# Performance work log

Hardware: AMD Instinct MI355X
Metric: run time of the kernel (lower is better)

Reference implementation:

```python
import jax, jax.numpy as jnp
import numpy as np

NEG_SLOPE = 0.2
LN_EPS = 1e-6

B, L, D, H = 32, 512, 256, 4
N = B * L
E = 65536
C = D  # per-head out channels (GATConv out_channels=d_model)


def setup_inputs() -> dict:
    key = jax.random.key(0)
    ks = jax.random.split(key, 10)
    s = 1.0 / np.sqrt(D)
    inputs = jax.random.normal(ks[0], (B, L, D), dtype=jnp.float32)
    edge_index = jax.random.randint(ks[1], (2, E), 0, N, dtype=jnp.int64)
    return {
        "inputs": inputs,
        "edge_index": edge_index,
        "ln_gamma": jnp.ones((D,), jnp.float32),
        "ln_beta": jnp.zeros((D,), jnp.float32),
        "W1": jax.random.normal(ks[2], (D, D), jnp.float32) * s,   # linear_before_gnn
        "b1": jnp.zeros((D,), jnp.float32),
        "W_gat": jax.random.normal(ks[3], (H * C, D), jnp.float32) * s,  # GATConv.lin (no bias)
        "att_src": jax.random.normal(ks[4], (H, C), jnp.float32) * s,
        "att_dst": jax.random.normal(ks[5], (H, C), jnp.float32) * s,
        "bias_gat": jnp.zeros((C,), jnp.float32),  # concat=False -> size out_channels
        "W2": jax.random.normal(ks[6], (D, D), jnp.float32) * s,   # linear_after_gnn
        "b2": jnp.zeros((D,), jnp.float32),
    }


def _gat_conv(x, edge_index, W_gat, att_src, att_dst, bias_gat):
    # x: [N, D] -> project to [N, H, C]
    xh = (x @ W_gat.T).reshape(N, H, C)
    # add self loops (PyG default add_self_loops=True)
    loops = jnp.arange(N, dtype=edge_index.dtype)
    src = jnp.concatenate([edge_index[0], loops])  # message source j
    dst = jnp.concatenate([edge_index[1], loops])  # message target i
    # per-node attention logits [N, H]
    a_src = jnp.einsum("nhc,hc->nh", xh, att_src)
    a_dst = jnp.einsum("nhc,hc->nh", xh, att_dst)
    # per-edge logits and segment softmax over destination node
    e = jax.nn.leaky_relu(a_src[src] + a_dst[dst], NEG_SLOPE)  # [Etot, H]
    e_max = jax.ops.segment_max(e, dst, num_segments=N)        # every node has a self loop
    e = jnp.exp(e - e_max[dst])
    denom = jax.ops.segment_sum(e, dst, num_segments=N)
    alpha = e / denom[dst]                                     # [Etot, H]
    # weighted message aggregation (dropout on alpha skipped: eval mode)
    msg = xh[src] * alpha[:, :, None]                          # [Etot, H, C]
    out = jax.ops.segment_sum(msg, dst, num_segments=N)        # [N, H, C]
    return out.mean(axis=1) + bias_gat                         # concat=False -> head mean


def reference(inputs, edge_index, ln_gamma, ln_beta, W1, b1, W_gat, att_src, att_dst, bias_gat, W2, b2):
    # LayerNorm(eps=1e-6)
    mu = inputs.mean(-1, keepdims=True)
    var = jnp.mean((inputs - mu) ** 2, axis=-1, keepdims=True)
    x = (inputs - mu) * jax.lax.rsqrt(var + LN_EPS) * ln_gamma + ln_beta
    x = x.reshape(-1, D)
    gnn_in = x @ W1.T + b1
    gnn_out = _gat_conv(gnn_in, edge_index, W_gat, att_src, att_dst, bias_gat)
    y = gnn_out @ W2.T + b2
    # dropout is identity in eval mode; residual add
    return y.reshape(B, L, D) + inputs
```

## Files before the change

kernel.cpp:

```cpp
#include <hip/hip_runtime.h>
#include <math.h>

#define N_NODES 16384
#define D_MODEL 256
#define H_HEADS 4
#define C_CH 256
#define E_EDGES 65536
#define ETOT (E_EDGES + N_NODES)
#define HC 1024
#define MAXDEG 64
#define PSZ 262144

typedef __bf16 bf16x8 __attribute__((ext_vector_type(8)));
typedef __bf16 bf16x4 __attribute__((ext_vector_type(4)));
typedef float f32x4 __attribute__((ext_vector_type(4)));

__device__ __forceinline__ __bf16 f2bf(float f) { return (__bf16)f; }
__device__ __forceinline__ float bf2f(__bf16 b) { return (float)b; }

__global__ __launch_bounds__(256) void prep1_ln(
    const float* __restrict__ Wg, const float* __restrict__ att_src,
    const float* __restrict__ att_dst, const float* __restrict__ W2,
    const int* __restrict__ ei, const float* __restrict__ in,
    const float* __restrict__ gamma, const float* __restrict__ beta,
    float* __restrict__ t, float* __restrict__ Vp, int* __restrict__ cnt,
    int* __restrict__ csr, __bf16* __restrict__ x_ln)
{
    int b = blockIdx.x;
    int tid = threadIdx.x;
    if (b >= 2432) {
        int wave = tid >> 6, lane = tid & 63;
        int row = (b - 2432) * 4 + wave;
        float4 v = ((const float4*)(in + (size_t)row * D_MODEL))[lane];
        float s  = v.x + v.y + v.z + v.w;
        float sq = v.x*v.x + v.y*v.y + v.z*v.z + v.w*v.w;
        for (int off = 32; off; off >>= 1) {
            s  += __shfl_xor(s,  off);
            sq += __shfl_xor(sq, off);
        }
        float mean = s * (1.0f / D_MODEL);
        float var  = sq * (1.0f / D_MODEL) - mean * mean;
        float inv  = rsqrtf(var + 1e-6f);
        float4 g = ((const float4*)gamma)[lane];
        float4 bb = ((const float4*)beta)[lane];
        bf16x4 o;
        o[0] = f2bf((v.x - mean) * inv * g.x + bb.x);
        o[1] = f2bf((v.y - mean) * inv * g.y + bb.y);
        o[2] = f2bf((v.z - mean) * inv * g.z + bb.z);
        o[3] = f2bf((v.w - mean) * inv * g.w + bb.w);
        *(bf16x4*)(x_ln + (size_t)row * D_MODEL + lane * 4) = o;
        return;
    }
    if (b < 64) {
        int v = b >> 3, sl = b & 7, h = v & 3;
        const float* att = ((v < 4) ? att_src : att_dst) + h * C_CH;
        float acc = 0.f;
        #pragma unroll
        for (int j = 0; j < 32; ++j) {
            int c = sl * 32 + j;
            acc = fmaf(Wg[(size_t)(h * 256 + c) * 256 + tid], att[c], acc);
        }
        atomicAdd(&t[v * 256 + tid], acc);
        return;
    }
    if (b < 2112) {
        int bb2 = b - 64;
        int orig = bb2 >> 3, cs = bb2 & 7;
        int og = (orig & 63) * 4, h = orig >> 6;
        const float* w2r = W2 + (size_t)og * 256;
        const float* wgp = Wg + ((size_t)h * 256) * 256 + tid;
        float a0 = 0.f, a1 = 0.f, a2 = 0.f, a3 = 0.f;
        int cb = cs * 32;
        #pragma unroll 4
        for (int c = cb; c < cb + 32; ++c) {
            float wv = wgp[(size_t)c * 256];
            a0 = fmaf(w2r[c],       wv, a0);
            a1 = fmaf(w2r[256 + c], wv, a1);
            a2 = fmaf(w2r[512 + c], wv, a2);
            a3 = fmaf(w2r[768 + c], wv, a3);
        }
        size_t base = (size_t)cs * PSZ + (size_t)og * 1024 + h * 256 + tid;
        Vp[base]        = a0;
        Vp[base + 1024] = a1;
        Vp[base + 2048] = a2;
        Vp[base + 3072] = a3;
        return;
    }
    {
        int e = (b - 2112) * 256 + tid;
        int src, dst;
        if (e < E_EDGES) { src = ei[e]; dst = ei[E_EDGES + e]; }
        else             { src = dst = e - E_EDGES; }
        int pos = atomicAdd(cnt + dst, 1);
        csr[(size_t)dst * MAXDEG + pos] = src;
    }
}

__global__ __launch_bounds__(256) void prep2(
    const float* __restrict__ t, const float* __restrict__ W1,
    const float* __restrict__ b1, const float* __restrict__ Vp,
    const float* __restrict__ W2, const float* __restrict__ bg,
    const float* __restrict__ b2, float* __restrict__ u2,
    float* __restrict__ c0, float* __restrict__ Wzp,
    float* __restrict__ bias_z)
{
    __shared__ float red[4][4];
    __shared__ float vsh[4][32];
    int b = blockIdx.x;
    int d = threadIdx.x;

    if (b < 2048) {
        int orig = b >> 3, ks = b & 7;
        int og = (orig & 63) * 4, h = orig >> 6;
        int lane = d & 63, wid = d >> 6;
        int kb = ks * 32;
        size_t vbase = (size_t)og * 1024 + h * 256;

        if (d < 128) {
            int j = d >> 5, kk = d & 31;
            float s = 0.f;
            #pragma unroll
            for (int cs = 0; cs < 8; ++cs)
                s += Vp[(size_t)cs * PSZ + vbase + (size_t)j * 1024 + kb + kk];
            vsh[j][kk] = s;
        }
        __syncthreads();

        float a0 = 0.f, a1 = 0.f, a2 = 0.f, a3 = 0.f;
        #pragma unroll 4
        for (int k = 0; k < 32; ++k) {
            float w1v = W1[(size_t)(kb + k) * 256 + d];
            a0 = fmaf(vsh[0][k], w1v, a0);
            a1 = fmaf(vsh[1][k], w1v, a1);
            a2 = fmaf(vsh[2][k], w1v, a2);
            a3 = fmaf(vsh[3][k], w1v, a3);
        }
        size_t base = (size_t)ks * PSZ + vbase + d;
        Wzp[base]        = a0;
        Wzp[base + 1024] = a1;
        Wzp[base + 2048] = a2;
        Wzp[base + 3072] = a3;

        if (ks == 0) {
            float b1v = b1[d];
            #pragma unroll
            for (int j = 0; j < 4; ++j) {
                float vsum = 0.f;
                #pragma unroll
                for (int cs = 0; cs < 8; ++cs)
                    vsum += Vp[(size_t)cs * PSZ + vbase + (size_t)j * 1024 + d];
                float p = vsum * b1v;
                for (int s = 32; s; s >>= 1) p += __shfl_xor(p, s);
                if (lane == 0) red[j][wid] = p;
            }
            __syncthreads();
            if (d < 4) {
                float s = red[d][0] + red[d][1] + red[d][2] + red[d][3];
                atomicAdd(&bias_z[og + d], 0.25f * s);
            }
            if (h == 0) {
                __syncthreads();
                float bgv = bg[d];
                #pragma unroll
                for (int j = 0; j < 4; ++j) {
                    float q = W2[(size_t)(og + j) * 256 + d] * bgv;
                    for (int s = 32; s; s >>= 1) q += __shfl_xor(q, s);
                    if (lane == 0) red[j][wid] = q;
                }
                __syncthreads();
                if (d < 4) {
                    float s = red[d][0] + red[d][1] + red[d][2] + red[d][3];
                    atomicAdd(&bias_z[og + d], s + b2[og + d]);
                }
            }
        }
        return;
    }
    {
        int bb = b - 2048;
        int v = bb >> 3, sl = bb & 7;
        const float* tv = t + v * 256;
        float acc = 0.f;
        #pragma unroll
        for (int j = 0; j < 32; ++j) {
            int k = sl * 32 + j;
            acc = fmaf(tv[k], W1[(size_t)k * 256 + d], acc);
        }
        atomicAdd(&u2[v * 256 + d], acc);
        if (d < 32) {
            float p = tv[sl * 32 + d] * b1[sl * 32 + d];
            for (int s = 16; s; s >>= 1) p += __shfl_xor(p, s);
            if (d == 0) atomicAdd(&c0[v], p);
        }
    }
}

__global__ __launch_bounds__(256) void logits_cvt(
    const __bf16* __restrict__ x_ln, const float* __restrict__ u2,
    const float* __restrict__ c0, float* __restrict__ a_src,
    float* __restrict__ a_dst, const float* __restrict__ Wzp,
    __bf16* __restrict__ Wz)
{
    int b = blockIdx.x;
    int tid = threadIdx.x;
    if (b >= 4096) {
        int idx = (b - 4096) * 256 + tid;
        float4 v = make_float4(0.f, 0.f, 0.f, 0.f);
        #pragma unroll
        for (int p = 0; p < 8; ++p) {
            float4 t4 = ((const float4*)(Wzp + (size_t)p * PSZ))[idx];
            v.x += t4.x; v.y += t4.y; v.z += t4.z; v.w += t4.w;
        }
        bf16x4 o;
        o[0] = f2bf(v.x); o[1] = f2bf(v.y); o[2] = f2bf(v.z); o[3] = f2bf(v.w);
        *(bf16x4*)(Wz + (size_t)idx * 4) = o;
        return;
    }
    __shared__ float u2s[8][256];
    __shared__ float c0s[8];
    #pragma unroll
    for (int k = 0; k < 8; ++k) u2s[k][tid] = u2[k * 256 + tid];
    if (tid < 8) c0s[tid] = c0[tid];
    __syncthreads();

    int wave = tid >> 6, lane = tid & 63;
    int n = b * 4 + wave;
    int v = lane >> 3, p = lane & 7;
    const __bf16* xp = x_ln + (size_t)n * D_MODEL + p * 32;
    const float*  up = &u2s[v][p * 32];
    float acc = 0.f;
    #pragma unroll
    for (int ti = 0; ti < 4; ++ti) {
        bf16x8 x = *(const bf16x8*)(xp + ti * 8);
        #pragma unroll
        for (int j = 0; j < 8; ++j)
            acc = fmaf(bf2f(x[j]), up[ti * 8 + j], acc);
    }
    acc += __shfl_xor(acc, 1);
    acc += __shfl_xor(acc, 2);
    acc += __shfl_xor(acc, 4);
    if (p == 0) {
        float o = acc + c0s[v];
        if (v < 4) a_src[n * H_HEADS + v] = o;
        else       a_dst[n * H_HEADS + (v - 4)] = o;
    }
}

__global__ __launch_bounds__(256) void gat_fused(
    const __bf16* __restrict__ x_ln, const float* __restrict__ a_src,
    const float* __restrict__ a_dst, const int* __restrict__ cnt,
    const int* __restrict__ csr, __bf16* __restrict__ agg)
{
    int wave = threadIdx.x >> 6, lane = threadIdx.x & 63;
    int i = blockIdx.x * 4 + wave;
    int deg = cnt[i];
    int sidx = csr[(size_t)i * MAXDEG + lane];
    float4 ad = *(const float4*)(a_dst + i * H_HEADS);

    float acc[4][4] = {};
    float sm0 = 0.f, sm1 = 0.f, sm2 = 0.f, sm3 = 0.f;

    int e = 0;
    for (; e + 4 <= deg; e += 4) {
        int s0 = __shfl(sidx, e);
        int s1 = __shfl(sidx, e + 1);
        int s2 = __shfl(sidx, e + 2);
        int s3 = __shfl(sidx, e + 3);
        float4 A0 = *(const float4*)(a_src + s0 * H_HEADS);
        float4 A1 = *(const float4*)(a_src + s1 * H_HEADS);
        float4 A2 = *(const float4*)(a_src + s2 * H_HEADS);
        float4 A3 = *(const float4*)(a_src + s3 * H_HEADS);
        bf16x4 X0 = *(const bf16x4*)(x_ln + (size_t)s0 * D_MODEL + lane * 4);
        bf16x4 X1 = *(const bf16x4*)(x_ln + (size_t)s1 * D_MODEL + lane * 4);
        bf16x4 X2 = *(const bf16x4*)(x_ln + (size_t)s2 * D_MODEL + lane * 4);
        bf16x4 X3 = *(const bf16x4*)(x_ln + (size_t)s3 * D_MODEL + lane * 4);

        float l[4][4] = {
            {A0.x + ad.x, A0.y + ad.y, A0.z + ad.z, A0.w + ad.w},
            {A1.x + ad.x, A1.y + ad.y, A1.z + ad.z, A1.w + ad.w},
            {A2.x + ad.x, A2.y + ad.y, A2.z + ad.z, A2.w + ad.w},
            {A3.x + ad.x, A3.y + ad.y, A3.z + ad.z, A3.w + ad.w}};
        float wgt[4][4];
        #pragma unroll
        for (int q = 0; q < 4; ++q)
            #pragma unroll
            for (int h = 0; h < 4; ++h) {
                float lv = l[q][h];
                lv = (lv > 0.f) ? lv : 0.2f * lv;
                wgt[q][h] = __expf(lv);
            }
        sm0 += wgt[0][0] + wgt[1][0] + wgt[2][0] + wgt[3][0];
        sm1 += wgt[0][1] + wgt[1][1] + wgt[2][1] + wgt[3][1];
        sm2 += wgt[0][2] + wgt[1][2] + wgt[2][2] + wgt[3][2];
        sm3 += wgt[0][3] + wgt[1][3] + wgt[2][3] + wgt[3][3];
        #pragma unroll
        for (int j = 0; j < 4; ++j) {
            float x0 = bf2f(X0[j]), x1 = bf2f(X1[j]);
            float x2 = bf2f(X2[j]), x3 = bf2f(X3[j]);
            #pragma unroll
            for (int h = 0; h < 4; ++h) {
                float a = acc[h][j];
                a = fmaf(wgt[0][h], x0, a);
                a = fmaf(wgt[1][h], x1, a);
                a = fmaf(wgt[2][h], x2, a);
                a = fmaf(wgt[3][h], x3, a);
                acc[h][j] = a;
            }
        }
    }
    for (; e < deg; ++e) {
        int s = __shfl(sidx, e);
        float4 as = *(const float4*)(a_src + s * H_HEADS);
        bf16x4 x = *(const bf16x4*)(x_ln + (size_t)s * D_MODEL + lane * 4);
        float l0 = as.x + ad.x, l1 = as.y + ad.y,
              l2 = as.z + ad.z, l3 = as.w + ad.w;
        l0 = (l0 > 0.f) ? l0 : 0.2f * l0;
        l1 = (l1 > 0.f) ? l1 : 0.2f * l1;
        l2 = (l2 > 0.f) ? l2 : 0.2f * l2;
        l3 = (l3 > 0.f) ? l3 : 0.2f * l3;
        float w0 = __expf(l0), w1 = __expf(l1);
        float w2 = __expf(l2), w3 = __expf(l3);
        sm0 += w0; sm1 += w1; sm2 += w2; sm3 += w3;
        #pragma unroll
        for (int j = 0; j < 4; ++j) {
            float xv = bf2f(x[j]);
            acc[0][j] = fmaf(w0, xv, acc[0][j]);
            acc[1][j] = fmaf(w1, xv, acc[1][j]);
            acc[2][j] = fmaf(w2, xv, acc[2][j]);
            acc[3][j] = fmaf(w3, xv, acc[3][j]);
        }
    }
    float sc[4] = {0.25f / sm0, 0.25f / sm1, 0.25f / sm2, 0.25f / sm3};
    #pragma unroll
    for (int h = 0; h < 4; ++h) {
        bf16x4 o;
        #pragma unroll
        for (int j = 0; j < 4; ++j) o[j] = f2bf(acc[h][j] * sc[h]);
        *(bf16x4*)(agg + (size_t)i * HC + h * 256 + lane * 4) = o;
    }
}

#define APAD 72

__global__ __launch_bounds__(512) void gemm_skinny(
    const __bf16* __restrict__ A, const __bf16* __restrict__ B,
    const float* __restrict__ bias, const float* __restrict__ resid,
    float* __restrict__ outf, int K)
{
    __shared__ __align__(16) __bf16 As[64 * APAD];
    __shared__ __align__(16) __bf16 Bs[256 * APAD];
    int tid  = threadIdx.x;
    int lane = tid & 63;
    int w    = tid >> 6;
    int quad = lane >> 4;
    int l16  = lane & 15;
    int m0 = blockIdx.x * 64;
    int n0 = w * 32;

    int srow = tid >> 3, sp = tid & 7;
    const __bf16* Ab = A + (size_t)(m0 + srow) * K + sp * 8;
    const __bf16* Bb = B + (size_t)srow * K + sp * 8;
    size_t rstride = (size_t)64 * K;

    f32x4 acc[4][2] = {};

    bf16x8 a0_, b0_[4];
    bf16x8 a1_, b1_[4];

    auto compute = [&]() {
        #pragma unroll
        for (int ks = 0; ks < 2; ++ks) {
            bf16x8 af[4], bfr[2];
            #pragma unroll
            for (int mt = 0; mt < 4; ++mt)
                af[mt] = *(const bf16x8*)(As + (mt * 16 + l16) * APAD
                                          + ks * 32 + quad * 8);
            #pragma unroll
            for (int nt = 0; nt < 2; ++nt)
                bfr[nt] = *(const bf16x8*)(Bs + (n0 + nt * 16 + l16) * APAD
                                           + ks * 32 + quad * 8);
            #pragma unroll
            for (int mt = 0; mt < 4; ++mt)
                #pragma unroll
                for (int nt = 0; nt < 2; ++nt)
                    acc[mt][nt] = __builtin_amdgcn_mfma_f32_16x16x32_bf16(
                        af[mt], bfr[nt], acc[mt][nt], 0, 0, 0);
        }
    };

    a0_ = *(const bf16x8*)(Ab);
    #pragma unroll
    for (int t = 0; t < 4; ++t)
        b0_[t] = *(const bf16x8*)(Bb + t * rstride);

    for (int kb = 0; kb < K; kb += 128) {
        {
            const __bf16* Ap = Ab + kb + 64;
            const __bf16* Bp = Bb + kb + 64;
            a1_ = *(const bf16x8*)(Ap);
            #pragma unroll
            for (int t = 0; t < 4; ++t)
                b1_[t] = *(const bf16x8*)(Bp + t * rstride);
        }
        __syncthreads();
        *(bf16x8*)(As + srow * APAD + sp * 8) = a0_;
        #pragma unroll
        for (int t = 0; t < 4; ++t)
            *(bf16x8*)(Bs + (srow + t * 64) * APAD + sp * 8) = b0_[t];
        __syncthreads();
        compute();

        if (kb + 128 < K) {
            const __bf16* Ap = Ab + kb + 128;
            const __bf16* Bp = Bb + kb + 128;
            a0_ = *(const bf16x8*)(Ap);
            #pragma unroll
            for (int t = 0; t < 4; ++t)
                b0_[t] = *(const bf16x8*)(Bp + t * rstride);
        }
        __syncthreads();
        *(bf16x8*)(As + srow * APAD + sp * 8) = a1_;
        #pragma unroll
        for (int t = 0; t < 4; ++t)
            *(bf16x8*)(Bs + (srow + t * 64) * APAD + sp * 8) = b1_[t];
        __syncthreads();
        compute();
    }

    #pragma unroll
    for (int nt = 0; nt < 2; ++nt) {
        int col = n0 + nt * 16 + l16;
        float bv = bias[col];
        #pragma unroll
        for (int mt = 0; mt < 4; ++mt) {
            int row = m0 + mt * 16 + quad * 4;
            #pragma unroll
            for (int r = 0; r < 4; ++r) {
                size_t off = (size_t)(row + r) * C_CH + col;
                outf[off] = acc[mt][nt][r] + bv + resid[off];
            }
        }
    }
}

extern "C" void kernel_launch(void* const* d_in, const int* in_sizes, int n_in,
                              void* d_out, int out_size, void* d_ws, size_t ws_size,
                              hipStream_t stream)
{
    const float* inp      = (const float*)d_in[0];
    const int*   ei       = (const int*)  d_in[1];
    const float* ln_gamma = (const float*)d_in[2];
    const float* ln_beta  = (const float*)d_in[3];
    const float* W1       = (const float*)d_in[4];
    const float* b1       = (const float*)d_in[5];
    const float* W_gat    = (const float*)d_in[6];
    const float* att_src  = (const float*)d_in[7];
    const float* att_dst  = (const float*)d_in[8];
    const float* bias_gat = (const float*)d_in[9];
    const float* W2       = (const float*)d_in[10];
    const float* b2       = (const float*)d_in[11];

    char* ws = (char*)d_ws;
    __bf16* x_ln_bf = (__bf16*)(ws);
    __bf16* agg_bf  = (__bf16*)(ws + (8ull  << 20));
    __bf16* Wz_b    = (__bf16*)(ws + (40ull << 20));
    float*  a_src_b = (float*)(ws + (41ull << 20));
    float*  a_dst_b = a_src_b + (size_t)N_NODES * H_HEADS;
    float*  t_vec   = (float*)(ws + (42ull << 20));
    float*  u2      = t_vec + 2048;
    float*  c0      = u2 + 2048;
    float*  bias_z  = c0 + 8;
    int*    cnt     = (int*)(bias_z + 256);
    int*    csr     = (int*)(ws + (45ull << 20));
    float*  Vp      = (float*)(ws + (49ull << 20));
    float*  Wzp     = (float*)(ws + (57ull << 20));

    size_t zbytes = (2048 + 2048 + 8 + 256) * sizeof(float)
                  + N_NODES * sizeof(int);
    hipMemsetAsync(t_vec, 0, zbytes, stream);

    prep1_ln<<<2432 + 4096, 256, 0, stream>>>(W_gat, att_src, att_dst, W2, ei,
                                              inp, ln_gamma, ln_beta,
                                              t_vec, Vp, cnt, csr, x_ln_bf);
    prep2<<<2112, 256, 0, stream>>>(t_vec, W1, b1, Vp, W2, bias_gat, b2,
                                    u2, c0, Wzp, bias_z);
    logits_cvt<<<4096 + 256, 256, 0, stream>>>(x_ln_bf, u2, c0,
                                               a_src_b, a_dst_b, Wzp, Wz_b);
    gat_fused<<<N_NODES / 4, 256, 0, stream>>>(x_ln_bf, a_src_b, a_dst_b,
                                               cnt, csr, agg_bf);
    gemm_skinny<<<N_NODES / 64, 512, 0, stream>>>(agg_bf, Wz_b, bias_z, inp,
                                                  (float*)d_out, HC);
}
```

Baseline: 155.5 us.

## Parallelize GAT edge weights across lanes and halve split-K partials in prep

```diff
diff --git a/kernel.cpp b/kernel.cpp
--- a/kernel.cpp
+++ b/kernel.cpp
@@ -28,9 +28,9 @@
 {
     int b = blockIdx.x;
     int tid = threadIdx.x;
-    if (b >= 2432) {
+    if (b >= 1408) {
         int wave = tid >> 6, lane = tid & 63;
-        int row = (b - 2432) * 4 + wave;
+        int row = (b - 1408) * 4 + wave;
         float4 v = ((const float4*)(in + (size_t)row * D_MODEL))[lane];
         float s  = v.x + v.y + v.z + v.w;
         float sq = v.x*v.x + v.y*v.y + v.z*v.z + v.w*v.w;
@@ -63,16 +63,16 @@
         atomicAdd(&t[v * 256 + tid], acc);
         return;
     }
-    if (b < 2112) {
+    if (b < 1088) {
         int bb2 = b - 64;
-        int orig = bb2 >> 3, cs = bb2 & 7;
+        int orig = bb2 >> 2, cs = bb2 & 3;
         int og = (orig & 63) * 4, h = orig >> 6;
         const float* w2r = W2 + (size_t)og * 256;
         const float* wgp = Wg + ((size_t)h * 256) * 256 + tid;
         float a0 = 0.f, a1 = 0.f, a2 = 0.f, a3 = 0.f;
-        int cb = cs * 32;
+        int cb = cs * 64;
         #pragma unroll 4
-        for (int c = cb; c < cb + 32; ++c) {
+        for (int c = cb; c < cb + 64; ++c) {
             float wv = wgp[(size_t)c * 256];
             a0 = fmaf(w2r[c],       wv, a0);
             a1 = fmaf(w2r[256 + c], wv, a1);
@@ -87,7 +87,7 @@
         return;
     }
     {
-        int e = (b - 2112) * 256 + tid;
+        int e = (b - 1088) * 256 + tid;
         int src, dst;
         if (e < E_EDGES) { src = ei[e]; dst = ei[E_EDGES + e]; }
         else             { src = dst = e - E_EDGES; }
@@ -105,22 +105,22 @@
     float* __restrict__ bias_z)
 {
     __shared__ float red[4][4];
-    __shared__ float vsh[4][32];
+    __shared__ float vsh[4][64];
     int b = blockIdx.x;
     int d = threadIdx.x;
 
-    if (b < 2048) {
-        int orig = b >> 3, ks = b & 7;
+    if (b < 1024) {
+        int orig = b >> 2, ks = b & 3;
         int og = (orig & 63) * 4, h = orig >> 6;
         int lane = d & 63, wid = d >> 6;
-        int kb = ks * 32;
+        int kb = ks * 64;
         size_t vbase = (size_t)og * 1024 + h * 256;
 
-        if (d < 128) {
-            int j = d >> 5, kk = d & 31;
+        {
+            int j = d >> 6, kk = d & 63;
             float s = 0.f;
             #pragma unroll
-            for (int cs = 0; cs < 8; ++cs)
+            for (int cs = 0; cs < 4; ++cs)
                 s += Vp[(size_t)cs * PSZ + vbase + (size_t)j * 1024 + kb + kk];
             vsh[j][kk] = s;
         }
@@ -128,7 +128,7 @@
 
         float a0 = 0.f, a1 = 0.f, a2 = 0.f, a3 = 0.f;
         #pragma unroll 4
-        for (int k = 0; k < 32; ++k) {
+        for (int k = 0; k < 64; ++k) {
             float w1v = W1[(size_t)(kb + k) * 256 + d];
             a0 = fmaf(vsh[0][k], w1v, a0);
             a1 = fmaf(vsh[1][k], w1v, a1);
@@ -147,7 +147,7 @@
             for (int j = 0; j < 4; ++j) {
                 float vsum = 0.f;
                 #pragma unroll
-                for (int cs = 0; cs < 8; ++cs)
+                for (int cs = 0; cs < 4; ++cs)
                     vsum += Vp[(size_t)cs * PSZ + vbase + (size_t)j * 1024 + d];
                 float p = vsum * b1v;
                 for (int s = 32; s; s >>= 1) p += __shfl_xor(p, s);
@@ -177,7 +177,7 @@
         return;
     }
     {
-        int bb = b - 2048;
+        int bb = b - 1024;
         int v = bb >> 3, sl = bb & 7;
         const float* tv = t + v * 256;
         float acc = 0.f;
@@ -207,7 +207,7 @@
         int idx = (b - 4096) * 256 + tid;
         float4 v = make_float4(0.f, 0.f, 0.f, 0.f);
         #pragma unroll
-        for (int p = 0; p < 8; ++p) {
+        for (int p = 0; p < 4; ++p) {
             float4 t4 = ((const float4*)(Wzp + (size_t)p * PSZ))[idx];
             v.x += t4.x; v.y += t4.y; v.z += t4.z; v.w += t4.w;
         }
@@ -251,86 +251,61 @@
     const float* __restrict__ a_dst, const int* __restrict__ cnt,
     const int* __restrict__ csr, __bf16* __restrict__ agg)
 {
+    __shared__ float wsh[4][MAXDEG][4];
     int wave = threadIdx.x >> 6, lane = threadIdx.x & 63;
     int i = blockIdx.x * 4 + wave;
     int deg = cnt[i];
     int sidx = csr[(size_t)i * MAXDEG + lane];
     float4 ad = *(const float4*)(a_dst + i * H_HEADS);
 
-    float acc[4][4] = {};
-    float sm0 = 0.f, sm1 = 0.f, sm2 = 0.f, sm3 = 0.f;
-
-    int e = 0;
-    for (; e + 4 <= deg; e += 4) {
-        int s0 = __shfl(sidx, e);
-        int s1 = __shfl(sidx, e + 1);
-        int s2 = __shfl(sidx, e + 2);
-        int s3 = __shfl(sidx, e + 3);
-        float4 A0 = *(const float4*)(a_src + s0 * H_HEADS);
-        float4 A1 = *(const float4*)(a_src + s1 * H_HEADS);
-        float4 A2 = *(const float4*)(a_src + s2 * H_HEADS);
-        float4 A3 = *(const float4*)(a_src + s3 * H_HEADS);
-        bf16x4 X0 = *(const bf16x4*)(x_ln + (size_t)s0 * D_MODEL + lane * 4);
-        bf16x4 X1 = *(const bf16x4*)(x_ln + (size_t)s1 * D_MODEL + lane * 4);
-        bf16x4 X2 = *(const bf16x4*)(x_ln + (size_t)s2 * D_MODEL + lane * 4);
-        bf16x4 X3 = *(const bf16x4*)(x_ln + (size_t)s3 * D_MODEL + lane * 4);
-
-        float l[4][4] = {
-            {A0.x + ad.x, A0.y + ad.y, A0.z + ad.z, A0.w + ad.w},
-            {A1.x + ad.x, A1.y + ad.y, A1.z + ad.z, A1.w + ad.w},
-            {A2.x + ad.x, A2.y + ad.y, A2.z + ad.z, A2.w + ad.w},
-            {A3.x + ad.x, A3.y + ad.y, A3.z + ad.z, A3.w + ad.w}};
-        float wgt[4][4];
-        #pragma unroll
-        for (int q = 0; q < 4; ++q)
-            #pragma unroll
-            for (int h = 0; h < 4; ++h) {
-                float lv = l[q][h];
-                lv = (lv > 0.f) ? lv : 0.2f * lv;
-                wgt[q][h] = __expf(lv);
-            }
-        sm0 += wgt[0][0] + wgt[1][0] + wgt[2][0] + wgt[3][0];
-        sm1 += wgt[0][1] + wgt[1][1] + wgt[2][1] + wgt[3][1];
-        sm2 += wgt[0][2] + wgt[1][2] + wgt[2][2] + wgt[3][2];
-        sm3 += wgt[0][3] + wgt[1][3] + wgt[2][3] + wgt[3][3];
-        #pragma unroll
-        for (int j = 0; j < 4; ++j) {
-            float x0 = bf2f(X0[j]), x1 = bf2f(X1[j]);
-            float x2 = bf2f(X2[j]), x3 = bf2f(X3[j]);
-            #pragma unroll
-            for (int h = 0; h < 4; ++h) {
-                float a = acc[h][j];
-                a = fmaf(wgt[0][h], x0, a);
-                a = fmaf(wgt[1][h], x1, a);
-                a = fmaf(wgt[2][h], x2, a);
-                a = fmaf(wgt[3][h], x3, a);
-                acc[h][j] = a;
-            }
-        }
-    }
-    for (; e < deg; ++e) {
-        int s = __shfl(sidx, e);
-        float4 as = *(const float4*)(a_src + s * H_HEADS);
-        bf16x4 x = *(const bf16x4*)(x_ln + (size_t)s * D_MODEL + lane * 4);
+    float4 wgt = make_float4(0.f, 0.f, 0.f, 0.f);
+    if (lane < deg) {
+        float4 as = *(const float4*)(a_src + sidx * H_HEADS);
         float l0 = as.x + ad.x, l1 = as.y + ad.y,
               l2 = as.z + ad.z, l3 = as.w + ad.w;
         l0 = (l0 > 0.f) ? l0 : 0.2f * l0;
         l1 = (l1 > 0.f) ? l1 : 0.2f * l1;
         l2 = (l2 > 0.f) ? l2 : 0.2f * l2;
         l3 = (l3 > 0.f) ? l3 : 0.2f * l3;
-        float w0 = __expf(l0), w1 = __expf(l1);
-        float w2 = __expf(l2), w3 = __expf(l3);
-        sm0 += w0; sm1 += w1; sm2 += w2; sm3 += w3;
-        #pragma unroll
-        for (int j = 0; j < 4; ++j) {
-            float xv = bf2f(x[j]);
-            acc[0][j] = fmaf(w0, xv, acc[0][j]);
-            acc[1][j] = fmaf(w1, xv, acc[1][j]);
-            acc[2][j] = fmaf(w2, xv, acc[2][j]);
-            acc[3][j] = fmaf(w3, xv, acc[3][j]);
-        }
-    }
-    float sc[4] = {0.25f / sm0, 0.25f / sm1, 0.25f / sm2, 0.25f / sm3};
+        wgt = make_float4(__expf(l0), __expf(l1), __expf(l2), __expf(l3));
+    }
+    float s0 = wgt.x, s1 = wgt.y, s2 = wgt.z, s3 = wgt.w;
+    #pragma unroll
+    for (int off = 32; off; off >>= 1) {
+        s0 += __shfl_xor(s0, off);
+        s1 += __shfl_xor(s1, off);
+        s2 += __shfl_xor(s2, off);
+        s3 += __shfl_xor(s3, off);
+    }
+    *(float4*)&wsh[wave][lane][0] = wgt;
+
+    float acc[4][4] = {};
+    for (int e0 = 0; e0 < deg; e0 += 8) {
+        bf16x4 X[8];
+        float4 W[8];
+        #pragma unroll
+        for (int j = 0; j < 8; ++j) {
+            int ee = e0 + j;
+            bool val = ee < deg;
+            int el = val ? ee : 0;
+            int s = __shfl(sidx, el);
+            X[j] = *(const bf16x4*)(x_ln + (size_t)s * D_MODEL + lane * 4);
+            float4 wv = *(const float4*)&wsh[wave][el][0];
+            W[j] = val ? wv : make_float4(0.f, 0.f, 0.f, 0.f);
+        }
+        #pragma unroll
+        for (int j = 0; j < 8; ++j) {
+            #pragma unroll
+            for (int d = 0; d < 4; ++d) {
+                float xv = bf2f(X[j][d]);
+                acc[0][d] = fmaf(W[j].x, xv, acc[0][d]);
+                acc[1][d] = fmaf(W[j].y, xv, acc[1][d]);
+                acc[2][d] = fmaf(W[j].z, xv, acc[2][d]);
+                acc[3][d] = fmaf(W[j].w, xv, acc[3][d]);
+            }
+        }
+    }
+    float sc[4] = {0.25f / s0, 0.25f / s1, 0.25f / s2, 0.25f / s3};
     #pragma unroll
     for (int h = 0; h < 4; ++h) {
         bf16x4 o;
@@ -479,10 +454,10 @@
                   + N_NODES * sizeof(int);
     hipMemsetAsync(t_vec, 0, zbytes, stream);
 
-    prep1_ln<<<2432 + 4096, 256, 0, stream>>>(W_gat, att_src, att_dst, W2, ei,
+    prep1_ln<<<1408 + 4096, 256, 0, stream>>>(W_gat, att_src, att_dst, W2, ei,
                                               inp, ln_gamma, ln_beta,
                                               t_vec, Vp, cnt, csr, x_ln_bf);
-    prep2<<<2112, 256, 0, stream>>>(t_vec, W1, b1, Vp, W2, bias_gat, b2,
+    prep2<<<1088, 256, 0, stream>>>(t_vec, W1, b1, Vp, W2, bias_gat, b2,
                                     u2, c0, Wzp, bias_z);
     logits_cvt<<<4096 + 256, 256, 0, stream>>>(x_ln_bf, u2, c0,
                                                a_src_b, a_dst_b, Wzp, Wz_b);
```

Result: no change. 155.6 us (+0.0%).
